# Performance work log

Measured on AMD Instinct MI355X. Metric: run time of the kernel, lower is better.

The kernel has to match this reference:

```python
import jax, jax.numpy as jnp
import numpy as np

H_STEP = 0.1  # diffusion step size h


def vector_layer(V, W):
    """V: [B, Cin, 9, N]; W: [Cout, Cin, 6].
    Faithful to torch vectorLayer: per component-group, conv1d with kernel
    covering the 3 group entries == contraction over (Cin, group), then the
    scalar result is broadcast back to the 3 group positions.
    Groups [0,3,6]->W[:,:,:3], [1,4,7]->W[:,:,3:6], [2,5,8]->W[:,:,3:6]."""
    o0 = jnp.einsum('bcgn,ocg->bon', V[:, :, (0, 3, 6), :], W[:, :, 0:3])
    o1 = jnp.einsum('bcgn,ocg->bon', V[:, :, (1, 4, 7), :], W[:, :, 3:6])
    o2 = jnp.einsum('bcgn,ocg->bon', V[:, :, (2, 5, 8), :], W[:, :, 3:6])
    S = jnp.stack([o0, o1, o2], axis=2)          # [B, Cout, 3, N]
    return jnp.tile(S, (1, 1, 3, 1))             # positions i get o_{i%3}


def vector_relu(V, Q):
    """Projection ReLU. V: [B, C, 9, N] viewed as [B, C, 3, 3(xyz), N];
    subtract the ReLU'd projection onto direction Q per 3-vector."""
    B, C, _, N = V.shape
    V5 = V.reshape(B, C, 3, 3, N)
    qnorm = jnp.linalg.norm(Q)
    Qb = (Q / qnorm)[None, None, None, :, None]
    T = jnp.sum(V5 * Q[None, None, None, :, None], axis=3, keepdims=True)
    W = V5 - jax.nn.relu(T / qnorm) * Qb
    return W.reshape(B, C, 9, N)


def double_vector_layer(x, K1, K2, Q):
    x = vector_relu(x, Q)
    x = vector_layer(x, K1)
    x = vector_relu(x, Q)
    x = vector_layer(x, K2)
    return vector_relu(x, Q)


def setup_inputs() -> dict:
    key = jax.random.key(0)
    ks = jax.random.split(key, 12)
    N, E = 8192, 65536
    nNin, nEin, nNopen, nEopen, nNclose, nlayer = 3, 1, 16, 1, 3, 5
    nopen = nNopen + 2 * nEopen   # 18
    nhid = 2 * nopen              # 36
    s = 0.05  # kernel scale for numerical stability over 5 layers
    return {
        'xnV': jax.random.normal(ks[0], (1, nNin, 9, N), jnp.float32),
        'xeV': jax.random.normal(ks[1], (1, nEin, 9, E), jnp.float32),
        'iInd': jax.random.randint(ks[2], (E,), 0, N),
        'jInd': jax.random.randint(ks[3], (E,), 0, N),
        'K1Nopen': s * jax.random.normal(ks[4], (nNopen, nNin, 6), jnp.float32),
        'K2Nopen': s * jax.random.normal(ks[5], (nNopen, nNopen, 6), jnp.float32),
        'K1Eopen': s * jax.random.normal(ks[6], (nEopen, nEin, 6), jnp.float32),
        'K2Eopen': s * jax.random.normal(ks[7], (nEopen, nEopen, 6), jnp.float32),
        'KE1': s * jax.random.normal(ks[8], (nlayer, nhid, nhid, 6), jnp.float32),
        'KE2': s * jax.random.normal(ks[9], (nlayer, nhid, nhid, 6), jnp.float32),
        'KNclose': s * jax.random.normal(ks[10], (nNclose, nopen, 6), jnp.float32),
        'Q': jax.random.normal(ks[11], (3,), jnp.float32),
    }


def reference(xnV, xeV, iInd, jInd, K1Nopen, K2Nopen, K1Eopen, K2Eopen,
              KE1, KE2, KNclose, Q):
    N = xnV.shape[-1]
    nopen = K2Nopen.shape[0] + 2 * K2Eopen.shape[0]

    def node_grad(x):   # node -> edge gather difference
        return x[..., iInd] - x[..., jInd]

    def node_ave(x):    # node -> edge gather average
        return 0.5 * (x[..., iInd] + x[..., jInd])

    def edge_div(g):    # edge -> node signed scatter-add
        z = jnp.zeros(g.shape[:-1] + (N,), g.dtype)
        return z.at[..., iInd].add(g).at[..., jInd].add(-g)

    def edge_ave(g):    # edge -> node averaged scatter-add
        z = jnp.zeros(g.shape[:-1] + (N,), g.dtype)
        return 0.5 * z.at[..., iInd].add(g).at[..., jInd].add(g)

    xn = double_vector_layer(xnV, K1Nopen, K2Nopen, Q)   # [1,16,9,N]
    xe = double_vector_layer(xeV, K1Eopen, K2Eopen, Q)   # [1,1,9,E]
    xn = jnp.concatenate([xn, edge_div(xe), edge_ave(xe)], axis=1)  # [1,18,9,N]

    Flux = None
    for i in range(KE1.shape[0]):  # fixed nlayer=5 structurally distinct weights
        dxe = jnp.concatenate([node_grad(xn), node_ave(xn)], axis=1)  # [1,36,9,E]
        Flux = double_vector_layer(dxe, KE1[i], KE2[i], Q)            # [1,36,9,E]
        dxn = edge_div(Flux[:, :nopen]) + edge_ave(Flux[:, nopen:])   # [1,18,9,N]
        xn = xn - H_STEP * dxn

    out = vector_layer(xn, KNclose)  # [1,3,9,N]
    return out, Flux
```

## Files before the change

### kernel.cpp

```cpp
#include <hip/hip_runtime.h>

#define N_NODES 8192
#define N_EDGES 65536
#define NS 56

#define XN3_OFF   0
#define MIT_OFF   (N_NODES*NS)
#define K2N_OFF   (MIT_OFF + 5*5760)
#define KNC_OFF   (K2N_OFF + 2*16*16)
#define K2E_OFF   (KNC_OFF + 2*3*18)
#define FLUX_OFF  488192
#define FLUX_END  (FLUX_OFF + 2*N_EDGES*56)
#define DEG_OFF   FLUX_END
#define RP_OFF    (DEG_OFF + N_NODES)
#define FP_OFF    (RP_OFF + N_NODES + 1)
#define POSI_OFF  (FP_OFF + N_NODES)
#define POSJ_OFF  (POSI_OFF + N_EDGES)

typedef float f32x2 __attribute__((ext_vector_type(2)));

template<int SLOT>
__device__ __forceinline__ float qb(float x) {
    int r = __builtin_amdgcn_update_dpp(0, __float_as_int(x), SLOT * 0x55, 0xf, 0xf, true);
    return __int_as_float(r);
}
__device__ __forceinline__ float qswap2(float x) {
    int r = __builtin_amdgcn_update_dpp(0, __float_as_int(x), 0x4E, 0xf, 0xf, true);
    return __int_as_float(r);
}

__device__ __forceinline__ void vrelu_p(float& a0, f32x2& a12,
                                        float q0, f32x2 q12, float iq2) {
    float t = fmaf(a0, q0, fmaf(a12.x, q12.x, a12.y * q12.y));
    float r = t > 0.f ? t * iq2 : 0.f;
    a0 = fmaf(-r, q0, a0);
    f32x2 nr = {-r, -r};
    a12 = nr * q12 + a12;
}

__device__ __forceinline__ void vrelu3(float& x0, float& x1, float& x2,
                                       float q0, float q1, float q2, float iq2) {
    float t = x0*q0 + x1*q1 + x2*q2;
    float r = t > 0.f ? t*iq2 : 0.f;
    x0 = fmaf(-r, q0, x0);
    x1 = fmaf(-r, q1, x1);
    x2 = fmaf(-r, q2, x2);
}

__device__ __forceinline__ void ld28(const float4* __restrict__ p, float (&d)[28]) {
#pragma unroll
    for (int t = 0; t < 7; ++t) {
        float4 r = p[t];
        d[4*t] = r.x; d[4*t+1] = r.y; d[4*t+2] = r.z; d[4*t+3] = r.w;
    }
}

template<int QS>
__device__ __forceinline__ void matvec_part(const float* __restrict__ mbase, int q,
        const float (&v0)[9], const f32x2 (&v12)[9],
        f32x2 (&a0p)[4], float& a0s, f32x2 (&a12)[9]) {
    const float* rb = mbase + QS*720 + q*20;
#pragma unroll
    for (int kc = 0; kc < 9; ++kc) {
        float b0 = qb<QS>(v0[kc]);
        f32x2 b12; b12.x = qb<QS>(v12[kc].x); b12.y = qb<QS>(v12[kc].y);
        f32x2 bb0 = {b0, b0};
        const float4* rp = (const float4*)(rb + kc*80);
        float4 R0 = rp[0], R1 = rp[1], R2 = rp[2], R3 = rp[3], R4 = rp[4];
        f32x2 m0p[4] = {{R0.x,R0.y},{R0.z,R0.w},{R1.x,R1.y},{R1.z,R1.w}};
        float mA[9] = {R2.z,R2.w,R3.x,R3.y,R3.z,R3.w,R4.x,R4.y,R4.z};
#pragma unroll
        for (int k = 0; k < 4; ++k) a0p[k] = m0p[k] * bb0 + a0p[k];
        a0s = fmaf(R2.x, b0, a0s);
#pragma unroll
        for (int k = 0; k < 9; ++k) {
            f32x2 mm = {mA[k], mA[k]};
            a12[k] = mm * b12 + a12[k];
        }
    }
}

__global__ void precompute_kernel(const float* __restrict__ K2N,
                                  const float* __restrict__ K2E,
                                  const float* __restrict__ KE1,
                                  const float* __restrict__ KE2,
                                  const float* __restrict__ KNc,
                                  float* __restrict__ ws,
                                  int* __restrict__ deg) {
    int tid = blockIdx.x * blockDim.x + threadIdx.x;
    int nthr = gridDim.x * blockDim.x;
    if (tid < N_NODES) deg[tid] = 0;
    for (int m = tid; m < 1440; m += nthr) {
        ws[MIT_OFF + m*20 + 9]  = 0.f;
        ws[MIT_OFF + m*20 + 19] = 0.f;
    }
    for (int m = tid; m < 5*1296; m += nthr) {
        int l = m / 1296, oc = m % 1296;
        int o = oc / 36, c = oc % 36;
        int qq = o / 9, k = o % 9;
        const float* p1 = KE1 + (size_t)(l*1296 + oc)*6;
        const float* p2 = KE2 + (size_t)(l*1296 + oc)*6;
        int base = MIT_OFF + l*5760 + (c*4 + qq)*20;
        ws[base + k]             = p1[0] + p1[1] + p1[2];
        ws[base + 10 + k]        = p1[3] + p1[4] + p1[5];
        ws[base + 2880 + k]      = p2[0] + p2[1] + p2[2];
        ws[base + 2880 + 10 + k] = p2[3] + p2[4] + p2[5];
    }
    for (int m = tid; m < 2*256; m += nthr) {
        int s = m / 256, oc = m % 256;
        const float* p = K2N + oc*6 + 3*s;
        ws[K2N_OFF + m] = p[0] + p[1] + p[2];
    }
    for (int m = tid; m < 2*54; m += nthr) {
        int s = m / 54, oc = m % 54;
        const float* p = KNc + oc*6 + 3*s;
        ws[KNC_OFF + m] = p[0] + p[1] + p[2];
    }
    if (tid < 2) {
        const float* p = K2E + 3*tid;
        ws[K2E_OFF + tid] = p[0] + p[1] + p[2];
    }
}

__global__ void count_kernel(const int* __restrict__ iInd, const int* __restrict__ jInd,
                             int* __restrict__ deg) {
    int e = blockIdx.x * blockDim.x + threadIdx.x;
    if (e >= N_EDGES) return;
    atomicAdd(&deg[iInd[e]], 1);
    atomicAdd(&deg[jInd[e]], 1);
}

__global__ void scan_kernel(const int* __restrict__ deg, int* __restrict__ rowptr,
                            int* __restrict__ fpos) {
    __shared__ int lds[256];
    int t = threadIdx.x;
    int base = t * 32;
    int s = 0;
#pragma unroll
    for (int k = 0; k < 32; ++k) s += deg[base + k];
    lds[t] = s;
    __syncthreads();
    if (t == 0) {
        int run = 0;
        for (int k = 0; k < 256; ++k) { int v = lds[k]; lds[k] = run; run += v; }
        rowptr[N_NODES] = run;
    }
    __syncthreads();
    int off = lds[t];
#pragma unroll
    for (int k = 0; k < 32; ++k) {
        rowptr[base + k] = off;
        fpos[base + k] = off;
        off += deg[base + k];
    }
}

__global__ void fill_kernel(const int* __restrict__ iInd, const int* __restrict__ jInd,
                            int* __restrict__ fpos,
                            int* __restrict__ posI, int* __restrict__ posJ) {
    int e = blockIdx.x * blockDim.x + threadIdx.x;
    if (e >= N_EDGES) return;
    posI[e] = atomicAdd(&fpos[iInd[e]], 1);
    posJ[e] = atomicAdd(&fpos[jInd[e]], 1);
}

__global__ void open_kernel(const float* __restrict__ xnV,
                            const float* __restrict__ xeV,
                            const float* __restrict__ Q,
                            const float* __restrict__ K1N,
                            const float* __restrict__ K1E,
                            const float* __restrict__ ws,
                            const int* __restrict__ posI, const int* __restrict__ posJ,
                            float* __restrict__ xn3,
                            float4* __restrict__ seslot) {
    float q0 = Q[0], q1 = Q[1], q2 = Q[2];
    float iq2 = 1.f / (q0*q0 + q1*q1 + q2*q2);

    if (blockIdx.x < 32) {
        int n = blockIdx.x * 256 + threadIdx.x;
        float R[3][9];
#pragma unroll
        for (int c = 0; c < 3; ++c)
#pragma unroll
            for (int p = 0; p < 9; ++p)
                R[c][p] = xnV[(c*9 + p)*N_NODES + n];
#pragma unroll
        for (int c = 0; c < 3; ++c)
#pragma unroll
            for (int v = 0; v < 3; ++v)
                vrelu3(R[c][3*v], R[c][3*v+1], R[c][3*v+2], q0, q1, q2, iq2);

        float s[16][3];
#pragma unroll
        for (int o = 0; o < 16; ++o) {
            float a0 = 0.f, a1 = 0.f, a2 = 0.f;
#pragma unroll
            for (int c = 0; c < 3; ++c)
#pragma unroll
                for (int g = 0; g < 3; ++g) {
                    a0 = fmaf(R[c][3*g + 0], K1N[(o*3 + c)*6 + g],     a0);
                    a1 = fmaf(R[c][3*g + 1], K1N[(o*3 + c)*6 + 3 + g], a1);
                    a2 = fmaf(R[c][3*g + 2], K1N[(o*3 + c)*6 + 3 + g], a2);
                }
            s[o][0] = a0; s[o][1] = a1; s[o][2] = a2;
        }
#pragma unroll
        for (int o = 0; o < 16; ++o)
            vrelu3(s[o][0], s[o][1], s[o][2], q0, q1, q2, iq2);

        float u[16][3];
#pragma unroll
        for (int o = 0; o < 16; ++o) {
            float a0 = 0.f, a1 = 0.f, a2 = 0.f;
#pragma unroll
            for (int c = 0; c < 16; ++c) {
                float m0 = ws[K2N_OFF + o*16 + c];
                float mA = ws[K2N_OFF + 256 + o*16 + c];
                a0 = fmaf(m0, s[c][0], a0);
                a1 = fmaf(mA, s[c][1], a1);
                a2 = fmaf(mA, s[c][2], a2);
            }
            u[o][0] = a0; u[o][1] = a1; u[o][2] = a2;
            vrelu3(u[o][0], u[o][1], u[o][2], q0, q1, q2, iq2);
        }

        float* dst = xn3 + n*NS;
#pragma unroll
        for (int o = 0; o < 16; ++o) {
            int base = (o/9)*28 + (o%9)*3;
#pragma unroll
            for (int g = 0; g < 3; ++g)
                dst[base + g] = u[o][g];
        }
        dst[27] = 0.f;
    } else {
        int e = (blockIdx.x - 32) * 256 + threadIdx.x;
        float R[9];
#pragma unroll
        for (int p = 0; p < 9; ++p) R[p] = xeV[p*N_EDGES + e];
#pragma unroll
        for (int v = 0; v < 3; ++v)
            vrelu3(R[3*v], R[3*v+1], R[3*v+2], q0, q1, q2, iq2);

        float s0 = 0.f, s1 = 0.f, s2 = 0.f;
#pragma unroll
        for (int g = 0; g < 3; ++g) {
            s0 = fmaf(R[3*g + 0], K1E[g],     s0);
            s1 = fmaf(R[3*g + 1], K1E[3 + g], s1);
            s2 = fmaf(R[3*g + 2], K1E[3 + g], s2);
        }
        vrelu3(s0, s1, s2, q0, q1, q2, iq2);
        s0 *= ws[K2E_OFF + 0];
        s1 *= ws[K2E_OFF + 1];
        s2 *= ws[K2E_OFF + 1];
        vrelu3(s0, s1, s2, q0, q1, q2, iq2);

        int pi = posI[e], pj = posJ[e];
        seslot[2*pi]     = make_float4(s0, s1, s2, 0.f);
        seslot[2*pi + 1] = make_float4(0.5f*s0, 0.5f*s1, 0.5f*s2, 0.f);
        seslot[2*pj]     = make_float4(-s0, -s1, -s2, 0.f);
        seslot[2*pj + 1] = make_float4(0.5f*s0, 0.5f*s1, 0.5f*s2, 0.f);
    }
}

__global__ void open_gather_kernel(const float4* __restrict__ seslot,
                                   const int* __restrict__ rowptr,
                                   float* __restrict__ xn3) {
    int n = blockIdx.x * blockDim.x + threadIdx.x;
    if (n >= N_NODES) return;
    int beg = rowptr[n], end = rowptr[n + 1];
    float d0 = 0.f, d1 = 0.f, d2 = 0.f, a0 = 0.f, a1 = 0.f, a2 = 0.f;
    for (int d = beg; d < end; ++d) {
        float4 dv = seslot[2*d];
        float4 av = seslot[2*d + 1];
        d0 += dv.x; d1 += dv.y; d2 += dv.z;
        a0 += av.x; a1 += av.y; a2 += av.z;
    }
    float* dst = xn3 + n*NS;
    dst[49] = d0; dst[50] = d1; dst[51] = d2;
    dst[52] = a0; dst[53] = a1; dst[54] = a2;
    dst[55] = 0.f;
}

template<bool WRITE_FLUX>
__global__ __launch_bounds__(256, 4) void edge_compute_kernel(
        const float* __restrict__ xn3,
        const int* __restrict__ iInd, const int* __restrict__ jInd,
        const int* __restrict__ posI, const int* __restrict__ posJ,
        const float* __restrict__ Q,
        const float* __restrict__ mitg,
        float* __restrict__ flux, float* __restrict__ fluxOut) {
    __shared__ float mit[5760];
    {
        const float4* s4 = (const float4*)mitg;
        float4* d4 = (float4*)mit;
        for (int t = threadIdx.x; t < 1440; t += 256) d4[t] = s4[t];
    }
    __syncthreads();

    int tid = blockIdx.x * 256 + threadIdx.x;
    int e = tid >> 2, q = tid & 3;
    float q0 = Q[0];
    f32x2 q12 = {Q[1], Q[2]};
    float iq2 = 1.f / (q0*q0 + q12.x*q12.x + q12.y*q12.y);
    int i = iInd[e], j = jInd[e];
    const float4* xi = (const float4*)(xn3 + i*NS + 28*(q & 1));
    const float4* xj = (const float4*)(xn3 + j*NS + 28*(q & 1));

    float A[28], B[28];
    ld28(xi, A);
    ld28(xj, B);

    bool isAve = q >= 2;
    float sA = isAve ? 0.5f :  1.f;
    float sB = isAve ? 0.5f : -1.f;
    float v0[9]; f32x2 v12[9];
#pragma unroll
    for (int k = 0; k < 9; ++k) {
        v0[k]    = fmaf(sA, A[3*k],   sB * B[3*k]);
        v12[k].x = fmaf(sA, A[3*k+1], sB * B[3*k+1]);
        v12[k].y = fmaf(sA, A[3*k+2], sB * B[3*k+2]);
        vrelu_p(v0[k], v12[k], q0, q12, iq2);
    }

    f32x2 a0p[4]; float a0s; f32x2 a12[9];
#pragma unroll
    for (int k = 0; k < 4; ++k) a0p[k] = (f32x2){0.f, 0.f};
    a0s = 0.f;
#pragma unroll
    for (int k = 0; k < 9; ++k) a12[k] = (f32x2){0.f, 0.f};
    matvec_part<0>(mit, q, v0, v12, a0p, a0s, a12);
    matvec_part<1>(mit, q, v0, v12, a0p, a0s, a12);
    matvec_part<2>(mit, q, v0, v12, a0p, a0s, a12);
    matvec_part<3>(mit, q, v0, v12, a0p, a0s, a12);
#pragma unroll
    for (int k = 0; k < 9; ++k) {
        float w0 = (k < 8) ? ((k & 1) ? a0p[k>>1].y : a0p[k>>1].x) : a0s;
        f32x2 w12 = a12[k];
        vrelu_p(w0, w12, q0, q12, iq2);
        v0[k] = w0; v12[k] = w12;
    }
#pragma unroll
    for (int k = 0; k < 4; ++k) a0p[k] = (f32x2){0.f, 0.f};
    a0s = 0.f;
#pragma unroll
    for (int k = 0; k < 9; ++k) a12[k] = (f32x2){0.f, 0.f};
    matvec_part<0>(mit + 2880, q, v0, v12, a0p, a0s, a12);
    matvec_part<1>(mit + 2880, q, v0, v12, a0p, a0s, a12);
    matvec_part<2>(mit + 2880, q, v0, v12, a0p, a0s, a12);
    matvec_part<3>(mit + 2880, q, v0, v12, a0p, a0s, a12);

    float w0[9]; f32x2 w12[9];
#pragma unroll
    for (int k = 0; k < 9; ++k) {
        w0[k] = (k < 8) ? ((k & 1) ? a0p[k>>1].y : a0p[k>>1].x) : a0s;
        w12[k] = a12[k];
        vrelu_p(w0[k], w12[k], q0, q12, iq2);
    }

    float selO = (q < 2) ? 1.f  : 0.5f;
    float selP = (q < 2) ? 0.5f : -1.f;
    float outv[28];
#pragma unroll
    for (int k = 0; k < 9; ++k) {
        float o0 = qswap2(w0[k]);
        float o1 = qswap2(w12[k].x);
        float o2 = qswap2(w12[k].y);
        outv[3*k]   = fmaf(selO, w0[k],    selP * o0);
        outv[3*k+1] = fmaf(selO, w12[k].x, selP * o1);
        outv[3*k+2] = fmaf(selO, w12[k].y, selP * o2);
    }
    outv[27] = 0.f;
    int slot = (q < 2) ? posI[e] : posJ[e];
    float4* frow = (float4*)(flux + (size_t)slot*56 + (q & 1)*28);
#pragma unroll
    for (int t = 0; t < 7; ++t)
        frow[t] = make_float4(outv[4*t], outv[4*t+1], outv[4*t+2], outv[4*t+3]);

    if (WRITE_FLUX) {
#pragma unroll
        for (int k = 0; k < 9; ++k) {
#pragma unroll
            for (int p = 0; p < 9; ++p) {
                float wv = (p % 3 == 0) ? w0[k] : (p % 3 == 1) ? w12[k].x : w12[k].y;
                fluxOut[((size_t)((9*q + k)*9 + p))*N_EDGES + e] = wv;
            }
        }
    }
}

__global__ __launch_bounds__(64) void node_gather_kernel(
        const float* __restrict__ flux,
        const int* __restrict__ rowptr,
        float* __restrict__ xn3) {
    int n = blockIdx.x;
    int l = threadIdx.x;
    if (l >= 56) return;
    int beg = rowptr[n], end = rowptr[n + 1];
    const float* p = flux + (size_t)beg * 56 + l;
    float acc = 0.f, acc2 = 0.f;
    int d = beg;
    for (; d + 2 <= end; d += 2) {
        acc  += p[0];
        acc2 += p[56];
        p += 112;
    }
    if (d < end) acc += p[0];
    acc += acc2;
    float* x = xn3 + n*NS + l;
    *x = fmaf(-0.1f, acc, *x);
}

__global__ void close_kernel(const float* __restrict__ xn3,
                             const float* __restrict__ ws,
                             float* __restrict__ out) {
    int n = blockIdx.x * blockDim.x + threadIdx.x;
    if (n >= N_NODES) return;
    const float* x = xn3 + n*NS;
    float o[3][3];
#pragma unroll
    for (int oo = 0; oo < 3; ++oo) {
        float a0 = 0.f, a1 = 0.f, a2 = 0.f;
#pragma unroll
        for (int c = 0; c < 18; ++c) {
            int xidx = (c/9)*28 + (c%9)*3;
            float m0 = ws[KNC_OFF + oo*18 + c];
            float mA = ws[KNC_OFF + 54 + oo*18 + c];
            a0 = fmaf(m0, x[xidx + 0], a0);
            a1 = fmaf(mA, x[xidx + 1], a1);
            a2 = fmaf(mA, x[xidx + 2], a2);
        }
        o[oo][0] = a0; o[oo][1] = a1; o[oo][2] = a2;
    }
#pragma unroll
    for (int oo = 0; oo < 3; ++oo)
#pragma unroll
        for (int p = 0; p < 9; ++p)
            out[(oo*9 + p)*N_NODES + n] = o[oo][p % 3];
}

extern "C" void kernel_launch(void* const* d_in, const int* in_sizes, int n_in,
                              void* d_out, int out_size, void* d_ws, size_t ws_size,
                              hipStream_t stream) {
    const float* xnV = (const float*)d_in[0];
    const float* xeV = (const float*)d_in[1];
    const int*   iInd = (const int*)d_in[2];
    const int*   jInd = (const int*)d_in[3];
    const float* K1N = (const float*)d_in[4];
    const float* K2N = (const float*)d_in[5];
    const float* K1E = (const float*)d_in[6];
    const float* K2E = (const float*)d_in[7];
    const float* KE1 = (const float*)d_in[8];
    const float* KE2 = (const float*)d_in[9];
    const float* KNc = (const float*)d_in[10];
    const float* Q   = (const float*)d_in[11];

    float* ws   = (float*)d_ws;
    float* xn3  = ws + XN3_OFF;
    float* flux = ws + FLUX_OFF;
    int* wsi    = (int*)d_ws;
    int* deg    = wsi + DEG_OFF;
    int* rowptr = wsi + RP_OFF;
    int* fpos   = wsi + FP_OFF;
    int* posI   = wsi + POSI_OFF;
    int* posJ   = wsi + POSJ_OFF;

    float* out  = (float*)d_out;
    float* fluxOut = out + 3*9*N_NODES;

    precompute_kernel<<<64, 256, 0, stream>>>(K2N, K2E, KE1, KE2, KNc, ws, deg);
    count_kernel<<<N_EDGES/256, 256, 0, stream>>>(iInd, jInd, deg);
    scan_kernel<<<1, 256, 0, stream>>>(deg, rowptr, fpos);
    fill_kernel<<<N_EDGES/256, 256, 0, stream>>>(iInd, jInd, fpos, posI, posJ);

    open_kernel<<<32 + N_EDGES/256, 256, 0, stream>>>(
        xnV, xeV, Q, K1N, K1E, ws, posI, posJ, xn3, (float4*)flux);
    open_gather_kernel<<<N_NODES/256, 256, 0, stream>>>((const float4*)flux, rowptr, xn3);

    for (int l = 0; l < 5; ++l) {
        const float* mitg = ws + MIT_OFF + l*5760;
        if (l == 4)
            edge_compute_kernel<true><<<N_EDGES*4/256, 256, 0, stream>>>(
                xn3, iInd, jInd, posI, posJ, Q, mitg, flux, fluxOut);
        else
            edge_compute_kernel<false><<<N_EDGES*4/256, 256, 0, stream>>>(
                xn3, iInd, jInd, posI, posJ, Q, mitg, flux, nullptr);
        node_gather_kernel<<<N_NODES, 64, 0, stream>>>(flux, rowptr, xn3);
    }

    close_kernel<<<N_NODES/256, 256, 0, stream>>>(xn3, ws, out);
}
```

Baseline: 307.3 us.

## Store per-edge flux slots as packed fp16 and halve open-stage slot size

```diff
diff --git a/kernel.cpp b/kernel.cpp
--- a/kernel.cpp
+++ b/kernel.cpp
@@ -9,8 +9,8 @@
 #define K2N_OFF   (MIT_OFF + 5*5760)
 #define KNC_OFF   (K2N_OFF + 2*16*16)
 #define K2E_OFF   (KNC_OFF + 2*3*18)
-#define FLUX_OFF  488192
-#define FLUX_END  (FLUX_OFF + 2*N_EDGES*56)
+#define FLUX_OFF  488176
+#define FLUX_END  (FLUX_OFF + 2*N_EDGES*32)
 #define DEG_OFF   FLUX_END
 #define RP_OFF    (DEG_OFF + N_NODES)
 #define FP_OFF    (RP_OFF + N_NODES + 1)
@@ -18,6 +18,12 @@
 #define POSJ_OFF  (POSI_OFF + N_EDGES)
 
 typedef float f32x2 __attribute__((ext_vector_type(2)));
+typedef __fp16 fp16x2 __attribute__((ext_vector_type(2)));
+
+__device__ __forceinline__ unsigned pkrtz(float a, float b) {
+    fp16x2 h = __builtin_amdgcn_cvt_pkrtz(a, b);
+    return *(unsigned*)&h;
+}
 
 template<int SLOT>
 __device__ __forceinline__ float qb(float x) {
@@ -255,11 +261,8 @@
         s2 *= ws[K2E_OFF + 1];
         vrelu3(s0, s1, s2, q0, q1, q2, iq2);
 
-        int pi = posI[e], pj = posJ[e];
-        seslot[2*pi]     = make_float4(s0, s1, s2, 0.f);
-        seslot[2*pi + 1] = make_float4(0.5f*s0, 0.5f*s1, 0.5f*s2, 0.f);
-        seslot[2*pj]     = make_float4(-s0, -s1, -s2, 0.f);
-        seslot[2*pj + 1] = make_float4(0.5f*s0, 0.5f*s1, 0.5f*s2, 0.f);
+        seslot[posI[e]] = make_float4( s0,  s1,  s2,  1.f);
+        seslot[posJ[e]] = make_float4(-s0, -s1, -s2, -1.f);
     }
 }
 
@@ -271,10 +274,10 @@
     int beg = rowptr[n], end = rowptr[n + 1];
     float d0 = 0.f, d1 = 0.f, d2 = 0.f, a0 = 0.f, a1 = 0.f, a2 = 0.f;
     for (int d = beg; d < end; ++d) {
-        float4 dv = seslot[2*d];
-        float4 av = seslot[2*d + 1];
-        d0 += dv.x; d1 += dv.y; d2 += dv.z;
-        a0 += av.x; a1 += av.y; a2 += av.z;
+        float4 v = seslot[d];
+        d0 += v.x; d1 += v.y; d2 += v.z;
+        float hs = 0.5f * v.w;
+        a0 = fmaf(hs, v.x, a0); a1 = fmaf(hs, v.y, a1); a2 = fmaf(hs, v.z, a2);
     }
     float* dst = xn3 + n*NS;
     dst[49] = d0; dst[50] = d1; dst[51] = d2;
@@ -289,7 +292,7 @@
         const int* __restrict__ posI, const int* __restrict__ posJ,
         const float* __restrict__ Q,
         const float* __restrict__ mitg,
-        float* __restrict__ flux, float* __restrict__ fluxOut) {
+        unsigned* __restrict__ flux16, float* __restrict__ fluxOut) {
     __shared__ float mit[5760];
     {
         const float4* s4 = (const float4*)mitg;
@@ -360,7 +363,7 @@
 
     float selO = (q < 2) ? 1.f  : 0.5f;
     float selP = (q < 2) ? 0.5f : -1.f;
-    float outv[28];
+    float outv[27];
 #pragma unroll
     for (int k = 0; k < 9; ++k) {
         float o0 = qswap2(w0[k]);
@@ -370,12 +373,17 @@
         outv[3*k+1] = fmaf(selO, w12[k].x, selP * o1);
         outv[3*k+2] = fmaf(selO, w12[k].y, selP * o2);
     }
-    outv[27] = 0.f;
+    unsigned pk[16];
+#pragma unroll
+    for (int t = 0; t < 13; ++t) pk[t] = pkrtz(outv[2*t], outv[2*t+1]);
+    pk[13] = pkrtz(outv[26], 0.f);
+    pk[14] = 0u; pk[15] = 0u;
     int slot = (q < 2) ? posI[e] : posJ[e];
-    float4* frow = (float4*)(flux + (size_t)slot*56 + (q & 1)*28);
-#pragma unroll
-    for (int t = 0; t < 7; ++t)
-        frow[t] = make_float4(outv[4*t], outv[4*t+1], outv[4*t+2], outv[4*t+3]);
+    uint4* dst = (uint4*)(flux16 + (size_t)slot*32 + (q & 1)*16);
+    dst[0] = make_uint4(pk[0],  pk[1],  pk[2],  pk[3]);
+    dst[1] = make_uint4(pk[4],  pk[5],  pk[6],  pk[7]);
+    dst[2] = make_uint4(pk[8],  pk[9],  pk[10], pk[11]);
+    dst[3] = make_uint4(pk[12], pk[13], pk[14], pk[15]);
 
     if (WRITE_FLUX) {
 #pragma unroll
@@ -390,25 +398,27 @@
 }
 
 __global__ __launch_bounds__(64) void node_gather_kernel(
-        const float* __restrict__ flux,
+        const __fp16* __restrict__ flux16,
         const int* __restrict__ rowptr,
         float* __restrict__ xn3) {
     int n = blockIdx.x;
     int l = threadIdx.x;
-    if (l >= 56) return;
     int beg = rowptr[n], end = rowptr[n + 1];
-    const float* p = flux + (size_t)beg * 56 + l;
+    const __fp16* p = flux16 + (size_t)beg * 64 + l;
     float acc = 0.f, acc2 = 0.f;
     int d = beg;
     for (; d + 2 <= end; d += 2) {
-        acc  += p[0];
-        acc2 += p[56];
-        p += 112;
-    }
-    if (d < end) acc += p[0];
+        acc  += (float)p[0];
+        acc2 += (float)p[64];
+        p += 128;
+    }
+    if (d < end) acc += (float)p[0];
     acc += acc2;
-    float* x = xn3 + n*NS + l;
-    *x = fmaf(-0.1f, acc, *x);
+    int m = l & 31;
+    if (m < 27) {
+        float* x = xn3 + n*NS + (l >> 5)*28 + m;
+        *x = fmaf(-0.1f, acc, *x);
+    }
 }
 
 __global__ void close_kernel(const float* __restrict__ xn3,
@@ -457,7 +467,8 @@
 
     float* ws   = (float*)d_ws;
     float* xn3  = ws + XN3_OFF;
-    float* flux = ws + FLUX_OFF;
+    unsigned* flux16 = (unsigned*)(ws + FLUX_OFF);
+    float4* se4 = (float4*)(ws + FLUX_OFF);
     int* wsi    = (int*)d_ws;
     int* deg    = wsi + DEG_OFF;
     int* rowptr = wsi + RP_OFF;
@@ -474,18 +485,18 @@
     fill_kernel<<<N_EDGES/256, 256, 0, stream>>>(iInd, jInd, fpos, posI, posJ);
 
     open_kernel<<<32 + N_EDGES/256, 256, 0, stream>>>(
-        xnV, xeV, Q, K1N, K1E, ws, posI, posJ, xn3, (float4*)flux);
-    open_gather_kernel<<<N_NODES/256, 256, 0, stream>>>((const float4*)flux, rowptr, xn3);
+        xnV, xeV, Q, K1N, K1E, ws, posI, posJ, xn3, se4);
+    open_gather_kernel<<<N_NODES/256, 256, 0, stream>>>(se4, rowptr, xn3);
 
     for (int l = 0; l < 5; ++l) {
         const float* mitg = ws + MIT_OFF + l*5760;
         if (l == 4)
             edge_compute_kernel<true><<<N_EDGES*4/256, 256, 0, stream>>>(
-                xn3, iInd, jInd, posI, posJ, Q, mitg, flux, fluxOut);
+                xn3, iInd, jInd, posI, posJ, Q, mitg, flux16, fluxOut);
         else
             edge_compute_kernel<false><<<N_EDGES*4/256, 256, 0, stream>>>(
-                xn3, iInd, jInd, posI, posJ, Q, mitg, flux, nullptr);
-        node_gather_kernel<<<N_NODES, 64, 0, stream>>>(flux, rowptr, xn3);
+                xn3, iInd, jInd, posI, posJ, Q, mitg, flux16, nullptr);
+        node_gather_kernel<<<N_NODES, 64, 0, stream>>>((const __fp16*)flux16, rowptr, xn3);
     }
 
     close_kernel<<<N_NODES/256, 256, 0, stream>>>(xn3, ws, out);
```

After: 281.9 us. 1.09x faster.
